# Kernel optimization log

Measured on AMD Instinct MI355X. Metric: run time of the kernel, lower is better.

The kernel has to match this reference:

```python
import jax, jax.numpy as jnp
import numpy as np

# IntConv2d config
IN_C, OUT_C, K, STRIDE, PAD = 64, 128, 3, 1, 1
BATCH, H, W = 64, 56, 56


def setup_inputs() -> dict:
    key = jax.random.key(0)
    k1, k2 = jax.random.split(key, 2)
    # int8 NHWC activations (values in [-128, 127])
    x = jax.random.randint(k1, (BATCH, H, W, IN_C), -128, 128, dtype=jnp.int32).astype(jnp.int8)
    # weight layout (O, kH, kW, I) exactly as in the torch module
    weight = jax.random.randint(k2, (OUT_C, K, K, IN_C), -128, 128, dtype=jnp.int32).astype(jnp.int8)
    # module initializes bias to zeros(int8)
    bias = jnp.zeros((OUT_C,), dtype=jnp.int8)
    return {"x": x, "weight": weight, "bias": bias}


def reference(x, weight, bias):
    # int8 conv with exact int32 accumulation (what int8conv_cuda computes),
    # NHWC activations, OHWI weights -> NHWC int32 output.
    y = jax.lax.conv_general_dilated(
        x.astype(jnp.int32),
        weight.astype(jnp.int32),
        window_strides=(STRIDE, STRIDE),
        padding=((PAD, PAD), (PAD, PAD)),
        dimension_numbers=("NHWC", "OHWI", "NHWC"),
    )
    # int8 bias broadcast-added over channel dim; promotes to int32
    return y + bias.astype(jnp.int32)
```

## Files before the change

kernel.cpp:

```cpp
#include <hip/hip_runtime.h>

typedef int int4v __attribute__((ext_vector_type(4)));

#define IN_C    64
#define OUT_C   128
#define KTOT    576
#define N_W     73728
#define N_OUT   25690112

#define PIXB    80
#define NTILES  3136

__global__ __launch_bounds__(256) void pack_w_kernel(const int* __restrict__ wgt,
                                                     unsigned int* __restrict__ w8) {
    int t = blockIdx.x * 256 + threadIdx.x;
    int d = t << 2;
    int byte = d & 15;
    int lane = (d >> 4) & 63;
    int ntk  = d >> 10;
    int nt   = ntk & 7;
    int kt   = ntk >> 3;
    int k = kt * 64 + ((lane >> 4) << 4) + byte;
    int n = nt * 16 + (lane & 15);
    int4v v = *(const int4v*)(wgt + n * KTOT + k);
    w8[t] = (v.x & 0xff) | ((v.y & 0xff) << 8) | ((v.z & 0xff) << 16)
          | ((unsigned int)v.w << 24);
}

__device__ __forceinline__ int pack4(int4v a) {
    return (a.x & 0xff) | ((a.y & 0xff) << 8) | ((a.z & 0xff) << 16) | (a.w << 24);
}

__global__ __launch_bounds__(256, 4) void conv_halo_kernel(const int* __restrict__ x32,
                                                           const char* __restrict__ w8,
                                                           const int* __restrict__ bias,
                                                           int* __restrict__ out) {
    __shared__ char hx[100 * PIXB];

    const int tid  = threadIdx.x;
    const int lane = tid & 63;
    const int wv   = tid >> 6;
    const int l15  = lane & 15;
    const int l4   = lane >> 4;

    const int bid = blockIdx.x;
    const int nb  = (bid & 7) * 392 + (bid >> 3);

    const int n   = nb / 49;
    const int rr  = nb - n * 49;
    const int th  = rr / 7;
    const int tw  = rr - th * 7;
    const int h0  = th * 8 - 1;
    const int w0  = tw * 8 - 1;

    const int pix0 = tid >> 2, q0 = tid & 3;
    const int hr0 = pix0 / 10, hc0 = pix0 - hr0 * 10;
    const bool has1 = tid < 144;
    const int pix1 = pix0 + 64;
    const int hr1 = pix1 / 10, hc1 = pix1 - hr1 * 10;

    int4v r00, r01, r02, r03, r10, r11, r12, r13;
    const int gh0 = h0 + hr0, gw0 = w0 + hc0;
    const bool ok0 = ((unsigned)gh0 < 56u) & ((unsigned)gw0 < 56u);
    if (ok0) {
        const int4v* s = (const int4v*)x32 + (((n * 56 + gh0) * 56 + gw0) << 4) + (q0 << 2);
        r00 = s[0]; r01 = s[1]; r02 = s[2]; r03 = s[3];
    }
    bool ok1 = false;
    if (has1) {
        int gh1 = h0 + hr1, gw1 = w0 + hc1;
        ok1 = ((unsigned)gh1 < 56u) & ((unsigned)gw1 < 56u);
        if (ok1) {
            const int4v* s = (const int4v*)x32 + (((n * 56 + gh1) * 56 + gw1) << 4) + (q0 << 2);
            r10 = s[0]; r11 = s[1]; r12 = s[2]; r13 = s[3];
        }
    }
    __builtin_amdgcn_sched_barrier(0);

    const char* wb = w8 + (((wv * 2) * 64 + lane) << 4);
    int4v bR[4][2];
#pragma unroll
    for (int i = 0; i < 4; ++i) {
        bR[i][0] = *(const int4v*)(wb);
        bR[i][1] = *(const int4v*)(wb + 1024);
        wb += 8192;
    }
    __builtin_amdgcn_sched_barrier(0);

    {
        int4v pk = {0, 0, 0, 0};
        if (ok0) { pk.x = pack4(r00); pk.y = pack4(r01); pk.z = pack4(r02); pk.w = pack4(r03); }
        *(int4v*)(hx + pix0 * PIXB + (q0 << 4)) = pk;
    }
    if (has1) {
        int4v pk = {0, 0, 0, 0};
        if (ok1) { pk.x = pack4(r10); pk.y = pack4(r11); pk.z = pack4(r12); pk.w = pack4(r13); }
        *(int4v*)(hx + pix1 * PIXB + (q0 << 4)) = pk;
    }
    __syncthreads();

    const char* ap = hx + ((l15 >> 3) * 10 + (l15 & 7)) * PIXB + (l4 << 4);

    int4v acc[4][2];
#pragma unroll
    for (int mt = 0; mt < 4; ++mt) {
        acc[mt][0] = (int4v){0, 0, 0, 0};
        acc[mt][1] = (int4v){0, 0, 0, 0};
    }

    int toff = 0;
#pragma unroll
    for (int kt = 0; kt < 9; ++kt) {
        int4v c0 = bR[kt & 3][0];
        int4v c1 = bR[kt & 3][1];
        if (kt < 5) {
            bR[kt & 3][0] = *(const int4v*)(wb);
            bR[kt & 3][1] = *(const int4v*)(wb + 1024);
            wb += 8192;
        }
#pragma unroll
        for (int mt = 0; mt < 4; ++mt) {
            int4v a = *(const int4v*)(ap + toff + mt * 1600);
            acc[mt][0] = __builtin_amdgcn_mfma_i32_16x16x64_i8(c0, a, acc[mt][0], 0, 0, 0);
            acc[mt][1] = __builtin_amdgcn_mfma_i32_16x16x64_i8(c1, a, acc[mt][1], 0, 0, 0);
        }
        toff += 80;
        if ((kt == 2) | (kt == 5)) toff += 560;
    }

    const int chb = wv * 32 + (l4 << 2);
    int4v bv0 = *(const int4v*)(bias + chb);
    int4v bv1 = *(const int4v*)(bias + chb + 16);
    int* ob = out + (((n * 56 + th * 8) * 56 + tw * 8) << 7);
    const int pc = l15 & 7;
    const int prl = l15 >> 3;
#pragma unroll
    for (int mt = 0; mt < 4; ++mt) {
        int pr = (mt << 1) + prl;
        int* o = ob + ((pr * 56 + pc) << 7) + chb;
        *(int4v*)(o)      = acc[mt][0] + bv0;
        *(int4v*)(o + 16) = acc[mt][1] + bv1;
    }
}

__global__ __launch_bounds__(256) void conv_naive_kernel(const int* __restrict__ x,
                                                         const int* __restrict__ wgt,
                                                         const int* __restrict__ bias,
                                                         int* __restrict__ out) {
    int idx = blockIdx.x * 256 + threadIdx.x;
    if (idx >= N_OUT) return;
    int ch  = idx & 127;
    int pix = idx >> 7;
    int n  = pix / 3136;
    int r2 = pix - n * 3136;
    int h  = r2 / 56;
    int w  = r2 - h * 56;
    int acc = bias[ch];
    for (int kh = 0; kh < 3; ++kh) {
        int hxr = h + kh - 1;
        if ((unsigned)hxr >= 56u) continue;
        for (int kw = 0; kw < 3; ++kw) {
            int wx = w + kw - 1;
            if ((unsigned)wx >= 56u) continue;
            const int* xp = x + ((n * 56 + hxr) * 56 + wx) * 64;
            const int* wp = wgt + ch * KTOT + (kh * 3 + kw) * 64;
            for (int ic = 0; ic < 64; ++ic) acc += xp[ic] * wp[ic];
        }
    }
    out[idx] = acc;
}

extern "C" void kernel_launch(void* const* d_in, const int* in_sizes, int n_in,
                              void* d_out, int out_size, void* d_ws, size_t ws_size,
                              hipStream_t stream) {
    const int* x    = (const int*)d_in[0];
    const int* wgt  = (const int*)d_in[1];
    const int* bias = (const int*)d_in[2];
    int* out = (int*)d_out;

    if (ws_size >= (size_t)N_W) {
        char* w8 = (char*)d_ws;
        pack_w_kernel<<<N_W / 4 / 256, 256, 0, stream>>>(wgt, (unsigned int*)w8);
        conv_halo_kernel<<<NTILES, 256, 0, stream>>>(x, w8, bias, out);
    } else {
        conv_naive_kernel<<<(N_OUT + 255) / 256, 256, 0, stream>>>(x, wgt, bias, out);
    }
}
```

Baseline: 39.99 us.

## Pre-pack activations to int8 and stage halo tiles via direct global-to-LDS loads

Adds a prep kernel that packs the int32 activations into an int8 buffer and also packs the weights. The conv kernel then loads the halo tile straight into LDS with global_load_lds, dropping the padded 80-byte pixel stride and the in-register packing. The aim is to cut the conv kernel's global read traffic and register pressure, which allows higher occupancy (launch bounds 5). The cost is an extra full pass that reads the 51 MB int32 input and writes a 12.8 MB int8 copy, plus possible LDS bank conflicts now that the pixel stride is 64 bytes.

```diff
diff --git a/kernel.cpp b/kernel.cpp
--- a/kernel.cpp
+++ b/kernel.cpp
@@ -5,37 +5,47 @@
 #define IN_C    64
 #define OUT_C   128
 #define KTOT    576
+#define N_X     12845056
 #define N_W     73728
 #define N_OUT   25690112
-
-#define PIXB    80
 #define NTILES  3136
 
-__global__ __launch_bounds__(256) void pack_w_kernel(const int* __restrict__ wgt,
-                                                     unsigned int* __restrict__ w8) {
-    int t = blockIdx.x * 256 + threadIdx.x;
-    int d = t << 2;
-    int byte = d & 15;
-    int lane = (d >> 4) & 63;
-    int ntk  = d >> 10;
-    int nt   = ntk & 7;
-    int kt   = ntk >> 3;
-    int k = kt * 64 + ((lane >> 4) << 4) + byte;
-    int n = nt * 16 + (lane & 15);
-    int4v v = *(const int4v*)(wgt + n * KTOT + k);
-    w8[t] = (v.x & 0xff) | ((v.y & 0xff) << 8) | ((v.z & 0xff) << 16)
-          | ((unsigned int)v.w << 24);
-}
+#define PW_BLKS 72
+#define PX_BLKS 12544
 
 __device__ __forceinline__ int pack4(int4v a) {
     return (a.x & 0xff) | ((a.y & 0xff) << 8) | ((a.z & 0xff) << 16) | (a.w << 24);
 }
 
-__global__ __launch_bounds__(256, 4) void conv_halo_kernel(const int* __restrict__ x32,
-                                                           const char* __restrict__ w8,
-                                                           const int* __restrict__ bias,
-                                                           int* __restrict__ out) {
-    __shared__ char hx[100 * PIXB];
+__global__ __launch_bounds__(256) void prep_kernel(const int* __restrict__ x,
+                                                   const int* __restrict__ wgt,
+                                                   unsigned int* __restrict__ x8,
+                                                   unsigned int* __restrict__ w8) {
+    const int bid = blockIdx.x;
+    if (bid < PW_BLKS) {
+        int t = bid * 256 + threadIdx.x;
+        int d = t << 2;
+        int byte = d & 15;
+        int lane = (d >> 4) & 63;
+        int ntk  = d >> 10;
+        int nt   = ntk & 7;
+        int kt   = ntk >> 3;
+        int k = kt * 64 + ((lane >> 4) << 4) + byte;
+        int n = nt * 16 + (lane & 15);
+        int4v v = *(const int4v*)(wgt + n * KTOT + k);
+        w8[t] = pack4(v);
+    } else {
+        int i = (bid - PW_BLKS) * 256 + threadIdx.x;
+        int4v v = ((const int4v*)x)[i];
+        x8[i] = pack4(v);
+    }
+}
+
+__global__ __launch_bounds__(256, 5) void conv_dma_kernel(const char* __restrict__ x8,
+                                                          const char* __restrict__ w8,
+                                                          const int* __restrict__ bias,
+                                                          int* __restrict__ out) {
+    __shared__ char hx[100 * 64];
 
     const int tid  = threadIdx.x;
     const int lane = tid & 63;
@@ -53,28 +63,38 @@
     const int h0  = th * 8 - 1;
     const int w0  = tw * 8 - 1;
 
-    const int pix0 = tid >> 2, q0 = tid & 3;
-    const int hr0 = pix0 / 10, hc0 = pix0 - hr0 * 10;
-    const bool has1 = tid < 144;
-    const int pix1 = pix0 + 64;
-    const int hr1 = pix1 / 10, hc1 = pix1 - hr1 * 10;
-
-    int4v r00, r01, r02, r03, r10, r11, r12, r13;
+    const int px0 = (wv << 4) + (lane >> 2);
+    const int q0  = lane & 3;
+    const int hr0 = px0 / 10, hc0 = px0 - hr0 * 10;
     const int gh0 = h0 + hr0, gw0 = w0 + hc0;
     const bool ok0 = ((unsigned)gh0 < 56u) & ((unsigned)gw0 < 56u);
-    if (ok0) {
-        const int4v* s = (const int4v*)x32 + (((n * 56 + gh0) * 56 + gw0) << 4) + (q0 << 2);
-        r00 = s[0]; r01 = s[1]; r02 = s[2]; r03 = s[3];
-    }
-    bool ok1 = false;
-    if (has1) {
-        int gh1 = h0 + hr1, gw1 = w0 + hc1;
-        ok1 = ((unsigned)gh1 < 56u) & ((unsigned)gw1 < 56u);
-        if (ok1) {
-            const int4v* s = (const int4v*)x32 + (((n * 56 + gh1) * 56 + gw1) << 4) + (q0 << 2);
-            r10 = s[0]; r11 = s[1]; r12 = s[2]; r13 = s[3];
-        }
-    }
+
+    const int unit1 = 256 + wv * 36 + lane;
+    const int px1 = unit1 >> 2;
+    const int hr1 = px1 / 10, hc1 = px1 - hr1 * 10;
+    const int gh1 = h0 + hr1, gw1 = w0 + hc1;
+    const bool ok1 = (lane < 36) & ((unsigned)gh1 < 56u) & ((unsigned)gw1 < 56u);
+
+    const bool border = (th == 0) | (th == 6) | (tw == 0) | (tw == 6);
+    if (border) {
+        int4v z = {0, 0, 0, 0};
+        *(int4v*)(hx + (((wv << 6) + lane) << 4)) = z;
+        if (lane < 36) *(int4v*)(hx + (unit1 << 4)) = z;
+        asm volatile("s_waitcnt lgkmcnt(0)" ::: "memory");
+    }
+
+    if (ok0)
+        __builtin_amdgcn_global_load_lds(
+            (const __attribute__((address_space(1))) void*)
+                (x8 + (((n * 3136 + gh0 * 56 + gw0) << 6) + (q0 << 4))),
+            (__attribute__((address_space(3))) void*)(hx + (wv << 10)),
+            16, 0, 0);
+    if (ok1)
+        __builtin_amdgcn_global_load_lds(
+            (const __attribute__((address_space(1))) void*)
+                (x8 + (((n * 3136 + gh1 * 56 + gw1) << 6) + (q0 << 4))),
+            (__attribute__((address_space(3))) void*)(hx + 4096 + wv * 576),
+            16, 0, 0);
     __builtin_amdgcn_sched_barrier(0);
 
     const char* wb = w8 + (((wv * 2) * 64 + lane) << 4);
@@ -87,19 +107,9 @@
     }
     __builtin_amdgcn_sched_barrier(0);
 
-    {
-        int4v pk = {0, 0, 0, 0};
-        if (ok0) { pk.x = pack4(r00); pk.y = pack4(r01); pk.z = pack4(r02); pk.w = pack4(r03); }
-        *(int4v*)(hx + pix0 * PIXB + (q0 << 4)) = pk;
-    }
-    if (has1) {
-        int4v pk = {0, 0, 0, 0};
-        if (ok1) { pk.x = pack4(r10); pk.y = pack4(r11); pk.z = pack4(r12); pk.w = pack4(r13); }
-        *(int4v*)(hx + pix1 * PIXB + (q0 << 4)) = pk;
-    }
     __syncthreads();
 
-    const char* ap = hx + ((l15 >> 3) * 10 + (l15 & 7)) * PIXB + (l4 << 4);
+    const char* ap = hx + (((l15 >> 3) * 10 + (l15 & 7)) << 6) + (l4 << 4);
 
     int4v acc[4][2];
 #pragma unroll
@@ -120,12 +130,12 @@
         }
 #pragma unroll
         for (int mt = 0; mt < 4; ++mt) {
-            int4v a = *(const int4v*)(ap + toff + mt * 1600);
+            int4v a = *(const int4v*)(ap + toff + mt * 1280);
             acc[mt][0] = __builtin_amdgcn_mfma_i32_16x16x64_i8(c0, a, acc[mt][0], 0, 0, 0);
             acc[mt][1] = __builtin_amdgcn_mfma_i32_16x16x64_i8(c1, a, acc[mt][1], 0, 0, 0);
         }
-        toff += 80;
-        if ((kt == 2) | (kt == 5)) toff += 560;
+        toff += 64;
+        if ((kt == 2) | (kt == 5)) toff += 448;
     }
 
     const int chb = wv * 32 + (l4 << 2);
@@ -178,10 +188,14 @@
     const int* bias = (const int*)d_in[2];
     int* out = (int*)d_out;
 
-    if (ws_size >= (size_t)N_W) {
-        char* w8 = (char*)d_ws;
-        pack_w_kernel<<<N_W / 4 / 256, 256, 0, stream>>>(wgt, (unsigned int*)w8);
-        conv_halo_kernel<<<NTILES, 256, 0, stream>>>(x, w8, bias, out);
+    const size_t need = (size_t)N_X + (size_t)N_W;
+    if (ws_size >= need) {
+        char* x8 = (char*)d_ws;
+        char* w8 = (char*)d_ws + N_X;
+        prep_kernel<<<PW_BLKS + PX_BLKS, 256, 0, stream>>>(x, wgt,
+                                                           (unsigned int*)x8,
+                                                           (unsigned int*)w8);
+        conv_dma_kernel<<<NTILES, 256, 0, stream>>>(x8, w8, bias, out);
     } else {
         conv_naive_kernel<<<(N_OUT + 255) / 256, 256, 0, stream>>>(x, wgt, bias, out);
     }
```

After: 51.84 us. +29.6%, slower.

## Process two vertically adjacent 8x8 tiles per block sharing a halo

Applied to the files above, without the earlier changes.

Each block now loads an 18x10 halo and computes two stacked 8x8 output tiles, except for the last tile row where a block handles a single tile. This cuts the halo re-read overhead and the per-block setup, and halves the block count. Weights are re-streamed from global memory for the second tile, and the second tile's MFMA work is serialized within the block. The larger LDS footprint and the uneven work between single- and double-tile blocks may reduce occupancy and balance.

```diff
diff --git a/kernel.cpp b/kernel.cpp
--- a/kernel.cpp
+++ b/kernel.cpp
@@ -9,7 +9,7 @@
 #define N_OUT   25690112
 
 #define PIXB    80
-#define NTILES  3136
+#define NBLKS   1792
 
 __global__ __launch_bounds__(256) void pack_w_kernel(const int* __restrict__ wgt,
                                                      unsigned int* __restrict__ w8) {
@@ -31,11 +31,11 @@
     return (a.x & 0xff) | ((a.y & 0xff) << 8) | ((a.z & 0xff) << 16) | (a.w << 24);
 }
 
-__global__ __launch_bounds__(256, 4) void conv_halo_kernel(const int* __restrict__ x32,
+__global__ __launch_bounds__(256, 4) void conv_pair_kernel(const int* __restrict__ x32,
                                                            const char* __restrict__ w8,
                                                            const int* __restrict__ bias,
                                                            int* __restrict__ out) {
-    __shared__ char hx[100 * PIXB];
+    __shared__ char hx[180 * PIXB];
 
     const int tid  = threadIdx.x;
     const int lane = tid & 63;
@@ -44,40 +44,48 @@
     const int l4   = lane >> 4;
 
     const int bid = blockIdx.x;
-    const int nb  = (bid & 7) * 392 + (bid >> 3);
-
-    const int n   = nb / 49;
-    const int rr  = nb - n * 49;
-    const int th  = rr / 7;
-    const int tw  = rr - th * 7;
-    const int h0  = th * 8 - 1;
+    const int nb  = (bid & 7) * 224 + (bid >> 3);
+
+    const int n   = nb / 28;
+    const int bp  = nb - n * 28;
+    const bool two = bp < 21;
+    const int th0 = two ? (bp / 7) * 2 : 6;
+    const int tw  = two ? (bp % 7) : (bp - 21);
+    const int h0  = th0 * 8 - 1;
     const int w0  = tw * 8 - 1;
 
-    const int pix0 = tid >> 2, q0 = tid & 3;
-    const int hr0 = pix0 / 10, hc0 = pix0 - hr0 * 10;
-    const bool has1 = tid < 144;
-    const int pix1 = pix0 + 64;
-    const int hr1 = pix1 / 10, hc1 = pix1 - hr1 * 10;
-
-    int4v r00, r01, r02, r03, r10, r11, r12, r13;
+    const int q = tid & 3;
+    const int px0 = tid >> 2;
+    const int hr0 = px0 / 10, hc0 = px0 - hr0 * 10;
+    const int px1 = px0 + 64;
+    const int hr1 = px1 / 10, hc1 = px1 - hr1 * 10;
+    const int px2 = px0 + 128;
+    const int hr2 = px2 / 10, hc2 = px2 - hr2 * 10;
+    const bool has2 = tid < 208;
+
+    int4v rA0, rA1, rA2, rA3, rB0, rB1, rB2, rB3, rC0, rC1, rC2, rC3;
     const int gh0 = h0 + hr0, gw0 = w0 + hc0;
     const bool ok0 = ((unsigned)gh0 < 56u) & ((unsigned)gw0 < 56u);
     if (ok0) {
-        const int4v* s = (const int4v*)x32 + (((n * 56 + gh0) * 56 + gw0) << 4) + (q0 << 2);
-        r00 = s[0]; r01 = s[1]; r02 = s[2]; r03 = s[3];
-    }
-    bool ok1 = false;
-    if (has1) {
-        int gh1 = h0 + hr1, gw1 = w0 + hc1;
-        ok1 = ((unsigned)gh1 < 56u) & ((unsigned)gw1 < 56u);
-        if (ok1) {
-            const int4v* s = (const int4v*)x32 + (((n * 56 + gh1) * 56 + gw1) << 4) + (q0 << 2);
-            r10 = s[0]; r11 = s[1]; r12 = s[2]; r13 = s[3];
-        }
+        const int4v* s = (const int4v*)x32 + (((n * 56 + gh0) * 56 + gw0) << 4) + (q << 2);
+        rA0 = s[0]; rA1 = s[1]; rA2 = s[2]; rA3 = s[3];
+    }
+    const int gh1 = h0 + hr1, gw1 = w0 + hc1;
+    const bool ok1 = ((unsigned)gh1 < 56u) & ((unsigned)gw1 < 56u);
+    if (ok1) {
+        const int4v* s = (const int4v*)x32 + (((n * 56 + gh1) * 56 + gw1) << 4) + (q << 2);
+        rB0 = s[0]; rB1 = s[1]; rB2 = s[2]; rB3 = s[3];
+    }
+    const int gh2 = h0 + hr2, gw2 = w0 + hc2;
+    const bool ok2 = has2 & ((unsigned)gh2 < 56u) & ((unsigned)gw2 < 56u);
+    if (ok2) {
+        const int4v* s = (const int4v*)x32 + (((n * 56 + gh2) * 56 + gw2) << 4) + (q << 2);
+        rC0 = s[0]; rC1 = s[1]; rC2 = s[2]; rC3 = s[3];
     }
     __builtin_amdgcn_sched_barrier(0);
 
-    const char* wb = w8 + (((wv * 2) * 64 + lane) << 4);
+    const char* wbase = w8 + (((wv * 2) * 64 + lane) << 4);
+    const char* wb = wbase;
     int4v bR[4][2];
 #pragma unroll
     for (int i = 0; i < 4; ++i) {
@@ -89,17 +97,27 @@
 
     {
         int4v pk = {0, 0, 0, 0};
-        if (ok0) { pk.x = pack4(r00); pk.y = pack4(r01); pk.z = pack4(r02); pk.w = pack4(r03); }
-        *(int4v*)(hx + pix0 * PIXB + (q0 << 4)) = pk;
-    }
-    if (has1) {
+        if (ok0) { pk.x = pack4(rA0); pk.y = pack4(rA1); pk.z = pack4(rA2); pk.w = pack4(rA3); }
+        *(int4v*)(hx + px0 * PIXB + (q << 4)) = pk;
+    }
+    {
         int4v pk = {0, 0, 0, 0};
-        if (ok1) { pk.x = pack4(r10); pk.y = pack4(r11); pk.z = pack4(r12); pk.w = pack4(r13); }
-        *(int4v*)(hx + pix1 * PIXB + (q0 << 4)) = pk;
+        if (ok1) { pk.x = pack4(rB0); pk.y = pack4(rB1); pk.z = pack4(rB2); pk.w = pack4(rB3); }
+        *(int4v*)(hx + px1 * PIXB + (q << 4)) = pk;
+    }
+    if (has2) {
+        int4v pk = {0, 0, 0, 0};
+        if (ok2) { pk.x = pack4(rC0); pk.y = pack4(rC1); pk.z = pack4(rC2); pk.w = pack4(rC3); }
+        *(int4v*)(hx + px2 * PIXB + (q << 4)) = pk;
     }
     __syncthreads();
 
-    const char* ap = hx + ((l15 >> 3) * 10 + (l15 & 7)) * PIXB + (l4 << 4);
+    const char* ap0 = hx + ((l15 >> 3) * 10 + (l15 & 7)) * PIXB + (l4 << 4);
+    const int chb = wv * 32 + (l4 << 2);
+    const int4v bv0 = *(const int4v*)(bias + chb);
+    const int4v bv1 = *(const int4v*)(bias + chb + 16);
+    const int pc = l15 & 7;
+    const int prl = l15 >> 3;
 
     int4v acc[4][2];
 #pragma unroll
@@ -107,7 +125,6 @@
         acc[mt][0] = (int4v){0, 0, 0, 0};
         acc[mt][1] = (int4v){0, 0, 0, 0};
     }
-
     int toff = 0;
 #pragma unroll
     for (int kt = 0; kt < 9; ++kt) {
@@ -120,7 +137,7 @@
         }
 #pragma unroll
         for (int mt = 0; mt < 4; ++mt) {
-            int4v a = *(const int4v*)(ap + toff + mt * 1600);
+            int4v a = *(const int4v*)(ap0 + toff + mt * 1600);
             acc[mt][0] = __builtin_amdgcn_mfma_i32_16x16x64_i8(c0, a, acc[mt][0], 0, 0, 0);
             acc[mt][1] = __builtin_amdgcn_mfma_i32_16x16x64_i8(c1, a, acc[mt][1], 0, 0, 0);
         }
@@ -128,18 +145,63 @@
         if ((kt == 2) | (kt == 5)) toff += 560;
     }
 
-    const int chb = wv * 32 + (l4 << 2);
-    int4v bv0 = *(const int4v*)(bias + chb);
-    int4v bv1 = *(const int4v*)(bias + chb + 16);
-    int* ob = out + (((n * 56 + th * 8) * 56 + tw * 8) << 7);
-    const int pc = l15 & 7;
-    const int prl = l15 >> 3;
-#pragma unroll
-    for (int mt = 0; mt < 4; ++mt) {
-        int pr = (mt << 1) + prl;
-        int* o = ob + ((pr * 56 + pc) << 7) + chb;
-        *(int4v*)(o)      = acc[mt][0] + bv0;
-        *(int4v*)(o + 16) = acc[mt][1] + bv1;
+    if (two) {
+        wb = wbase;
+#pragma unroll
+        for (int i = 0; i < 4; ++i) {
+            bR[i][0] = *(const int4v*)(wb);
+            bR[i][1] = *(const int4v*)(wb + 1024);
+            wb += 8192;
+        }
+    }
+    __builtin_amdgcn_sched_barrier(0);
+
+    {
+        int* ob = out + (((n * 56 + th0 * 8) * 56 + tw * 8) << 7);
+#pragma unroll
+        for (int mt = 0; mt < 4; ++mt) {
+            int pr = (mt << 1) + prl;
+            int* o = ob + ((pr * 56 + pc) << 7) + chb;
+            *(int4v*)(o)      = acc[mt][0] + bv0;
+            *(int4v*)(o + 16) = acc[mt][1] + bv1;
+        }
+    }
+
+    if (two) {
+        const char* ap1 = ap0 + 8 * 800;
+#pragma unroll
+        for (int mt = 0; mt < 4; ++mt) {
+            acc[mt][0] = (int4v){0, 0, 0, 0};
+            acc[mt][1] = (int4v){0, 0, 0, 0};
+        }
+        toff = 0;
+#pragma unroll
+        for (int kt = 0; kt < 9; ++kt) {
+            int4v c0 = bR[kt & 3][0];
+            int4v c1 = bR[kt & 3][1];
+            if (kt < 5) {
+                bR[kt & 3][0] = *(const int4v*)(wb);
+                bR[kt & 3][1] = *(const int4v*)(wb + 1024);
+                wb += 8192;
+            }
+#pragma unroll
+            for (int mt = 0; mt < 4; ++mt) {
+                int4v a = *(const int4v*)(ap1 + toff + mt * 1600);
+                acc[mt][0] = __builtin_amdgcn_mfma_i32_16x16x64_i8(c0, a, acc[mt][0], 0, 0, 0);
+                acc[mt][1] = __builtin_amdgcn_mfma_i32_16x16x64_i8(c1, a, acc[mt][1], 0, 0, 0);
+            }
+            toff += 80;
+            if ((kt == 2) | (kt == 5)) toff += 560;
+        }
+
+        int* ob = out + (((n * 56 + (th0 + 1) * 8) * 56 + tw * 8) << 7);
+#pragma unroll
+        for (int mt = 0; mt < 4; ++mt) {
+            int pr = (mt << 1) + prl;
+            int* o = ob + ((pr * 56 + pc) << 7) + chb;
+            *(int4v*)(o)      = acc[mt][0] + bv0;
+            *(int4v*)(o + 16) = acc[mt][1] + bv1;
+        }
     }
 }
 
@@ -178,10 +240,10 @@
     const int* bias = (const int*)d_in[2];
     int* out = (int*)d_out;
 
-    if (ws_size >= (size_t)N_W) {
+    if (ws_size >= (size_t)(N_W + 8192)) {
         char* w8 = (char*)d_ws;
         pack_w_kernel<<<N_W / 4 / 256, 256, 0, stream>>>(wgt, (unsigned int*)w8);
-        conv_halo_kernel<<<NTILES, 256, 0, stream>>>(x, w8, bias, out);
+        conv_pair_kernel<<<NBLKS, 256, 0, stream>>>(x, w8, bias, out);
     } else {
         conv_naive_kernel<<<(N_OUT + 255) / 256, 256, 0, stream>>>(x, wgt, bias, out);
     }
```

New measurement: 43.04 us. +7.6%, slower.

## Split conv tile across eight waves with 16 output channels each

Applied to the files above, without the earlier changes.

Blocks grow from 256 to 512 threads. Each wave now computes one 16-channel output tile instead of two, which halves the accumulators and weight registers per wave. The halo load is spread over 400 threads with one pixel-quarter each, replacing the previous two-per-thread scheme. The aim is higher occupancy and more latency hiding from lower register pressure, at the cost of each wave re-reading the shared-memory A fragments per channel tile, which doubles LDS read traffic.

```diff
diff --git a/kernel.cpp b/kernel.cpp
--- a/kernel.cpp
+++ b/kernel.cpp
@@ -31,10 +31,10 @@
     return (a.x & 0xff) | ((a.y & 0xff) << 8) | ((a.z & 0xff) << 16) | (a.w << 24);
 }
 
-__global__ __launch_bounds__(256, 4) void conv_halo_kernel(const int* __restrict__ x32,
-                                                           const char* __restrict__ w8,
-                                                           const int* __restrict__ bias,
-                                                           int* __restrict__ out) {
+__global__ __launch_bounds__(512, 5) void conv_8w_kernel(const int* __restrict__ x32,
+                                                         const char* __restrict__ w8,
+                                                         const int* __restrict__ bias,
+                                                         int* __restrict__ out) {
     __shared__ char hx[100 * PIXB];
 
     const int tid  = threadIdx.x;
@@ -53,94 +53,69 @@
     const int h0  = th * 8 - 1;
     const int w0  = tw * 8 - 1;
 
-    const int pix0 = tid >> 2, q0 = tid & 3;
-    const int hr0 = pix0 / 10, hc0 = pix0 - hr0 * 10;
-    const bool has1 = tid < 144;
-    const int pix1 = pix0 + 64;
-    const int hr1 = pix1 / 10, hc1 = pix1 - hr1 * 10;
-
-    int4v r00, r01, r02, r03, r10, r11, r12, r13;
-    const int gh0 = h0 + hr0, gw0 = w0 + hc0;
-    const bool ok0 = ((unsigned)gh0 < 56u) & ((unsigned)gw0 < 56u);
-    if (ok0) {
-        const int4v* s = (const int4v*)x32 + (((n * 56 + gh0) * 56 + gw0) << 4) + (q0 << 2);
-        r00 = s[0]; r01 = s[1]; r02 = s[2]; r03 = s[3];
-    }
-    bool ok1 = false;
-    if (has1) {
-        int gh1 = h0 + hr1, gw1 = w0 + hc1;
-        ok1 = ((unsigned)gh1 < 56u) & ((unsigned)gw1 < 56u);
-        if (ok1) {
-            const int4v* s = (const int4v*)x32 + (((n * 56 + gh1) * 56 + gw1) << 4) + (q0 << 2);
-            r10 = s[0]; r11 = s[1]; r12 = s[2]; r13 = s[3];
+    const int px0 = tid >> 2, q0 = tid & 3;
+    const int hr0 = px0 / 10, hc0 = px0 - hr0 * 10;
+    const bool hasu = tid < 400;
+    int4v r0, r1, r2, r3;
+    bool ok0 = false;
+    if (hasu) {
+        int gh = h0 + hr0, gw = w0 + hc0;
+        ok0 = ((unsigned)gh < 56u) & ((unsigned)gw < 56u);
+        if (ok0) {
+            const int4v* s = (const int4v*)x32 + (((n * 56 + gh) * 56 + gw) << 4) + (q0 << 2);
+            r0 = s[0]; r1 = s[1]; r2 = s[2]; r3 = s[3];
         }
     }
     __builtin_amdgcn_sched_barrier(0);
 
-    const char* wb = w8 + (((wv * 2) * 64 + lane) << 4);
-    int4v bR[4][2];
+    const char* wb = w8 + (wv << 10) + (lane << 4);
+    int4v bR[4];
 #pragma unroll
     for (int i = 0; i < 4; ++i) {
-        bR[i][0] = *(const int4v*)(wb);
-        bR[i][1] = *(const int4v*)(wb + 1024);
+        bR[i] = *(const int4v*)wb;
         wb += 8192;
     }
     __builtin_amdgcn_sched_barrier(0);
 
-    {
+    if (hasu) {
         int4v pk = {0, 0, 0, 0};
-        if (ok0) { pk.x = pack4(r00); pk.y = pack4(r01); pk.z = pack4(r02); pk.w = pack4(r03); }
-        *(int4v*)(hx + pix0 * PIXB + (q0 << 4)) = pk;
-    }
-    if (has1) {
-        int4v pk = {0, 0, 0, 0};
-        if (ok1) { pk.x = pack4(r10); pk.y = pack4(r11); pk.z = pack4(r12); pk.w = pack4(r13); }
-        *(int4v*)(hx + pix1 * PIXB + (q0 << 4)) = pk;
+        if (ok0) { pk.x = pack4(r0); pk.y = pack4(r1); pk.z = pack4(r2); pk.w = pack4(r3); }
+        *(int4v*)(hx + px0 * PIXB + (q0 << 4)) = pk;
     }
     __syncthreads();
 
     const char* ap = hx + ((l15 >> 3) * 10 + (l15 & 7)) * PIXB + (l4 << 4);
 
-    int4v acc[4][2];
-#pragma unroll
-    for (int mt = 0; mt < 4; ++mt) {
-        acc[mt][0] = (int4v){0, 0, 0, 0};
-        acc[mt][1] = (int4v){0, 0, 0, 0};
-    }
-
+    int4v acc0 = {0,0,0,0}, acc1 = {0,0,0,0}, acc2 = {0,0,0,0}, acc3 = {0,0,0,0};
     int toff = 0;
 #pragma unroll
     for (int kt = 0; kt < 9; ++kt) {
-        int4v c0 = bR[kt & 3][0];
-        int4v c1 = bR[kt & 3][1];
+        int4v c = bR[kt & 3];
         if (kt < 5) {
-            bR[kt & 3][0] = *(const int4v*)(wb);
-            bR[kt & 3][1] = *(const int4v*)(wb + 1024);
+            bR[kt & 3] = *(const int4v*)wb;
             wb += 8192;
         }
-#pragma unroll
-        for (int mt = 0; mt < 4; ++mt) {
-            int4v a = *(const int4v*)(ap + toff + mt * 1600);
-            acc[mt][0] = __builtin_amdgcn_mfma_i32_16x16x64_i8(c0, a, acc[mt][0], 0, 0, 0);
-            acc[mt][1] = __builtin_amdgcn_mfma_i32_16x16x64_i8(c1, a, acc[mt][1], 0, 0, 0);
-        }
+        int4v a0 = *(const int4v*)(ap + toff);
+        int4v a1 = *(const int4v*)(ap + toff + 1600);
+        int4v a2 = *(const int4v*)(ap + toff + 3200);
+        int4v a3 = *(const int4v*)(ap + toff + 4800);
+        acc0 = __builtin_amdgcn_mfma_i32_16x16x64_i8(c, a0, acc0, 0, 0, 0);
+        acc1 = __builtin_amdgcn_mfma_i32_16x16x64_i8(c, a1, acc1, 0, 0, 0);
+        acc2 = __builtin_amdgcn_mfma_i32_16x16x64_i8(c, a2, acc2, 0, 0, 0);
+        acc3 = __builtin_amdgcn_mfma_i32_16x16x64_i8(c, a3, acc3, 0, 0, 0);
         toff += 80;
         if ((kt == 2) | (kt == 5)) toff += 560;
     }
 
-    const int chb = wv * 32 + (l4 << 2);
-    int4v bv0 = *(const int4v*)(bias + chb);
-    int4v bv1 = *(const int4v*)(bias + chb + 16);
-    int* ob = out + (((n * 56 + th * 8) * 56 + tw * 8) << 7);
+    const int chb = (wv << 4) + (l4 << 2);
+    const int4v bv = *(const int4v*)(bias + chb);
+    int* ob = out + (((n * 56 + th * 8) * 56 + tw * 8) << 7) + chb;
     const int pc = l15 & 7;
     const int prl = l15 >> 3;
-#pragma unroll
-    for (int mt = 0; mt < 4; ++mt) {
-        int pr = (mt << 1) + prl;
-        int* o = ob + ((pr * 56 + pc) << 7) + chb;
-        *(int4v*)(o)      = acc[mt][0] + bv0;
-        *(int4v*)(o + 16) = acc[mt][1] + bv1;
-    }
+    *(int4v*)(ob + (((0 + prl) * 56 + pc) << 7)) = acc0 + bv;
+    *(int4v*)(ob + (((2 + prl) * 56 + pc) << 7)) = acc1 + bv;
+    *(int4v*)(ob + (((4 + prl) * 56 + pc) << 7)) = acc2 + bv;
+    *(int4v*)(ob + (((6 + prl) * 56 + pc) << 7)) = acc3 + bv;
 }
 
 __global__ __launch_bounds__(256) void conv_naive_kernel(const int* __restrict__ x,
@@ -181,7 +156,7 @@
     if (ws_size >= (size_t)N_W) {
         char* w8 = (char*)d_ws;
         pack_w_kernel<<<N_W / 4 / 256, 256, 0, stream>>>(wgt, (unsigned int*)w8);
-        conv_halo_kernel<<<NTILES, 256, 0, stream>>>(x, w8, bias, out);
+        conv_8w_kernel<<<NTILES, 512, 0, stream>>>(x, w8, bias, out);
     } else {
         conv_naive_kernel<<<(N_OUT + 255) / 256, 256, 0, stream>>>(x, wgt, bias, out);
     }
```

Result: slower. 43.39 us (+8.5%).
